# Kernel optimization log

Measured on AMD Instinct MI355X. Metric: run time of the kernel, lower is better.

Reference implementation:

```python
import jax, jax.numpy as jnp
import numpy as np

B, N, D = 2, 2048, 1024
H, QH, DH = 8, 16, 64        # kv heads, query heads, head dim
SOFTCLAMP = 50.0


def setup_inputs() -> dict:
    key = jax.random.key(0)
    ks = jax.random.split(key, 7)
    return {
        "tokens": jax.random.normal(ks[0], (B, N, D), jnp.float32),
        "norm_w": jnp.ones((D,), jnp.float32) + 0.02 * jax.random.normal(ks[1], (D,), jnp.float32),
        "Wq":  0.02 * jax.random.normal(ks[2], (D, QH * DH), jnp.float32),
        "Wkv": 0.02 * jax.random.normal(ks[3], (D, 2 * H * DH), jnp.float32),
        "Wout": 0.02 * jax.random.normal(ks[4], (H * DH, D), jnp.float32),
        "q_gamma": 0.02 * jax.random.normal(ks[5], (QH, DH), jnp.float32),
        "k_gamma": 0.02 * jax.random.normal(ks[6], (H, DH), jnp.float32),
    }


def _rmsnorm(x, w):
    eps = jnp.finfo(x.dtype).eps
    return x * jax.lax.rsqrt(jnp.mean(x * x, axis=-1, keepdims=True) + eps) * w


def _l2norm(x):
    # F.normalize(dim=-1, p=2) clamps the norm at eps=1e-12
    n = jnp.maximum(jnp.linalg.norm(x, axis=-1, keepdims=True), 1e-12)
    return x / n


def _mh_rmsnorm(x, gamma):
    # x: [b, h, n, d]; gamma: [h, d]; scale = (gamma + 1) * sqrt(d)
    scale = (gamma + 1.0) * np.sqrt(x.shape[-1]).astype(np.float32)
    return _l2norm(x) * scale[None, :, None, :]


def reference(tokens, norm_w, Wq, Wkv, Wout, q_gamma, k_gamma):
    b, n, d = tokens.shape
    x = _rmsnorm(tokens, norm_w)

    q = (x @ Wq).reshape(b, n, QH, DH).transpose(0, 2, 1, 3)      # [b, QH, n, dh]
    kv = x @ Wkv
    k = kv[..., : H * DH].reshape(b, n, H, DH).transpose(0, 2, 1, 3)  # [b, H, n, dh]
    v = kv[..., H * DH:].reshape(b, n, H, DH).transpose(0, 2, 1, 3)   # [b, H, n, dh]

    q = _mh_rmsnorm(q, q_gamma)
    k = _mh_rmsnorm(k, k_gamma)

    g = QH // H
    q = q.reshape(b, H, g, n, DH)                                 # [b, h, g, i, dh]

    sim = jnp.einsum('bhgid,bhjd->bhgij', q, k)                   # [b, h, g, i, j]
    sim = jnp.tanh(sim / SOFTCLAMP) * SOFTCLAMP                   # softcap BEFORE scale (faithful)
    sim = sim * (DH ** -0.5)

    neg = -jnp.finfo(sim.dtype).max
    causal = jnp.triu(jnp.ones((n, n), dtype=bool), 1)
    sim = jnp.where(causal, neg, sim)

    attn = jax.nn.softmax(sim, axis=-1)
    # NOTE: original einsum sums over the group axis g -> [b, h, i, dh]
    out = jnp.einsum('bhgij,bhjd->bhid', attn, v)
    out = out.transpose(0, 2, 1, 3).reshape(b, n, H * DH)
    return out @ Wout
```

## Files before the change

### kernel.cpp

```cpp
#include <hip/hip_runtime.h>
#include <hip/hip_bf16.h>
#include <type_traits>

typedef unsigned short u16;
typedef __attribute__((ext_vector_type(2))) float f32x2;
typedef __attribute__((ext_vector_type(4))) float f32x4;
typedef __attribute__((ext_vector_type(8))) short short8;
typedef __attribute__((ext_vector_type(4))) short short4v;
typedef __attribute__((ext_vector_type(8))) __bf16 bf16x8;
typedef __attribute__((ext_vector_type(4))) __bf16 bf16x4;

#define BB 2
#define NN 2048
#define DDIM 1024
#define HH 8
#define QHH 16
#define DHH 64

__device__ __forceinline__ float b2f(u16 v) {
    return __builtin_bit_cast(float, ((unsigned)v) << 16);
}
__device__ __forceinline__ u16 f2b(float f) {
    unsigned u = __builtin_bit_cast(unsigned, f);
    u += 0x7FFFu + ((u >> 16) & 1u);
    return (u16)(u >> 16);
}
__device__ __forceinline__ float fastrcp(float x) {
#if __has_builtin(__builtin_amdgcn_rcpf)
    return __builtin_amdgcn_rcpf(x);
#else
    return 1.0f / x;
#endif
}
__device__ __forceinline__ float fastexp2(float x) {
#if __has_builtin(__builtin_amdgcn_exp2f)
    return __builtin_amdgcn_exp2f(x);
#else
    return exp2f(x);
#endif
}
__device__ __forceinline__ f32x2 sp2(float v) { return (f32x2){v, v}; }
__device__ __forceinline__ f32x4 mfma16(short8 a, short8 b, f32x4 c) {
    return __builtin_amdgcn_mfma_f32_16x16x32_bf16(
        __builtin_bit_cast(bf16x8, a), __builtin_bit_cast(bf16x8, b), c, 0, 0, 0);
}
#if __has_builtin(__builtin_amdgcn_mfma_f32_16x16x16_bf16)
__device__ __forceinline__ f32x4 mfma_k16(short4v a, short4v b, f32x4 c) {
    return __builtin_amdgcn_mfma_f32_16x16x16_bf16(
        __builtin_bit_cast(bf16x4, a), __builtin_bit_cast(bf16x4, b), c, 0, 0, 0);
}
#else
__device__ __forceinline__ f32x4 mfma_k16(short4v a, short4v b, f32x4 c) {
    return __builtin_amdgcn_mfma_f32_16x16x16bf16_1k(a, b, c, 0, 0, 0);
}
#endif
__device__ __forceinline__ void stage16(const u16* g, u16* l, int lane) {
#if __has_builtin(__builtin_amdgcn_global_load_lds)
    __builtin_amdgcn_global_load_lds(
        (const __attribute__((address_space(1))) unsigned int*)g,
        (__attribute__((address_space(3))) unsigned int*)l, 16, 0, 0);
#else
    *(short8*)(l + lane * 8) = *(const short8*)g;
#endif
}

__global__ __launch_bounds__(256) void k_pre(const float* __restrict__ tokens,
                                             const float* __restrict__ norm_w,
                                             u16* __restrict__ xb,
                                             const float* __restrict__ Wq,
                                             const float* __restrict__ Wkv,
                                             const float* __restrict__ Wout,
                                             u16* __restrict__ WqT,
                                             u16* __restrict__ WkvT,
                                             u16* __restrict__ WoutT) {
    __shared__ float red[4];
    __shared__ u16 tile[32][33];
    const int bid = blockIdx.x;
    const int tid = threadIdx.x;
    if (bid < 4096) {
        const int row = bid;
        const float* xp = tokens + (size_t)row * DDIM + tid * 4;
        float4 raw = *(const float4*)xp;
        float ss = raw.x * raw.x + raw.y * raw.y + raw.z * raw.z + raw.w * raw.w;
#pragma unroll
        for (int d = 1; d < 64; d <<= 1) ss += __shfl_xor(ss, d);
        if ((tid & 63) == 0) red[tid >> 6] = ss;
        __syncthreads();
        float tot = red[0] + red[1] + red[2] + red[3];
        float r = rsqrtf(tot * (1.0f / 1024.0f) + 1.1920929e-7f);
        float4 wv = *(const float4*)(norm_w + tid * 4);
        ushort4 o;
        o.x = f2b(raw.x * r * wv.x);
        o.y = f2b(raw.y * r * wv.y);
        o.z = f2b(raw.z * r * wv.z);
        o.w = f2b(raw.w * r * wv.w);
        *(ushort4*)(xb + (size_t)row * DDIM + tid * 4) = o;
    } else {
        const int idx = bid - 4096;
        const int z = idx >> 10;
        const int rem = idx & 1023;
        const int by = rem >> 5, bx = rem & 31;
        const float* in = (z == 0) ? Wq : (z == 1) ? Wkv : Wout;
        u16* out = (z == 0) ? WqT : (z == 1) ? WkvT : WoutT;
        const int R = (z == 2) ? 512 : 1024, C = 1024;
        const int br = by * 32;
        if (br >= R) return;
        const int bc = bx * 32;
        const int tx = tid & 31, ty = tid >> 5;
#pragma unroll
        for (int i = 0; i < 32; i += 8)
            tile[ty + i][tx] = f2b(in[(size_t)(br + ty + i) * C + bc + tx]);
        __syncthreads();
#pragma unroll
        for (int i = 0; i < 32; i += 8)
            out[(size_t)(bc + ty + i) * R + br + tx] = tile[tx][ty + i];
    }
}

__global__ __launch_bounds__(256) void k_gemm128(const u16* __restrict__ A,
                                                 const u16* __restrict__ Bt,
                                                 u16* __restrict__ C,
                                                 int M, int Ncols, int K) {
    __shared__ __attribute__((aligned(16))) u16 As[128 * 64];
    __shared__ __attribute__((aligned(16))) u16 Bs[128 * 64];
    const int tid = threadIdx.x;
    const int lane = tid & 63;
    const int w = tid >> 6;
    const int i = blockIdx.y * 16 + blockIdx.x;
    const int xcd = i & 7, j = i >> 3;
    const int rm = xcd >> 1, rn = xcd & 1;
    const int m0 = (rm * 8 + (j >> 3)) * 128;
    const int n0 = (rn * 8 + (j & 7)) * 128;
    const int wr = (w >> 1) * 64;
    const int wc = (w & 1) * 64;
    const int lr = lane & 15;
    const int lq = lane >> 4;

    const int ch0 = w * 32;
    const int srow = lane >> 3;
    const int sch = (lane ^ srow) & 7;
    const u16* aSrc = A + (size_t)(m0 + ch0 + srow) * K + sch * 8;
    const u16* bSrc = Bt + (size_t)(n0 + ch0 + srow) * K + sch * 8;
    u16* aDst = As + ch0 * 64;
    u16* bDst = Bs + ch0 * 64;

    f32x4 acc[4][4];
#pragma unroll
    for (int i2 = 0; i2 < 4; i2++)
#pragma unroll
        for (int j2 = 0; j2 < 4; j2++) acc[i2][j2] = (f32x4){0.f, 0.f, 0.f, 0.f};

    for (int k0 = 0; k0 < K; k0 += 64) {
        __syncthreads();
#pragma unroll
        for (int c = 0; c < 4; ++c) {
            stage16(aSrc + (size_t)(c * 8) * K, aDst + c * 8 * 64, lane);
            stage16(bSrc + (size_t)(c * 8) * K, bDst + c * 8 * 64, lane);
        }
        aSrc += 64;
        bSrc += 64;
        __syncthreads();
#pragma unroll
        for (int kk = 0; kk < 2; ++kk) {
            short8 a[4], b[4];
#pragma unroll
            for (int mi = 0; mi < 4; ++mi) {
                const int row = wr + mi * 16 + lr;
                a[mi] = *(const short8*)&As[row * 64 + ((((kk << 2) + lq) ^ (lr & 7)) << 3)];
            }
#pragma unroll
            for (int ni = 0; ni < 4; ++ni) {
                const int row = wc + ni * 16 + lr;
                b[ni] = *(const short8*)&Bs[row * 64 + ((((kk << 2) + lq) ^ (lr & 7)) << 3)];
            }
#pragma unroll
            for (int mi = 0; mi < 4; ++mi)
#pragma unroll
                for (int ni = 0; ni < 4; ++ni) acc[mi][ni] = mfma16(a[mi], b[ni], acc[mi][ni]);
        }
    }
#pragma unroll
    for (int mi = 0; mi < 4; ++mi)
#pragma unroll
        for (int ni = 0; ni < 4; ++ni)
#pragma unroll
            for (int r = 0; r < 4; ++r) {
                int row = m0 + wr + mi * 16 + lq * 4 + r;
                int col = n0 + wc + ni * 16 + lr;
                C[(size_t)row * Ncols + col] = f2b(acc[mi][ni][r]);
            }
}

__global__ __launch_bounds__(256) void k_gemm64f(const u16* __restrict__ A,
                                                 const u16* __restrict__ Bt,
                                                 float* __restrict__ C,
                                                 int M, int Ncols, int K) {
    __shared__ __attribute__((aligned(16))) u16 As[64 * 64];
    __shared__ __attribute__((aligned(16))) u16 Bs[128 * 64];
    const int tid = threadIdx.x;
    const int lane = tid & 63;
    const int w = tid >> 6;
    const int m0 = blockIdx.y * 64;
    const int n0 = blockIdx.x * 128;
    const int lr = lane & 15;
    const int lq = lane >> 4;

    const int srow = lane >> 3;
    const int sch = (lane ^ srow) & 7;
    const u16* aSrc = A + (size_t)(m0 + w * 16 + srow) * K + sch * 8;
    const u16* bSrc = Bt + (size_t)(n0 + w * 32 + srow) * K + sch * 8;
    u16* aDst = As + w * 16 * 64;
    u16* bDst = Bs + w * 32 * 64;

    f32x4 acc[8];
#pragma unroll
    for (int i = 0; i < 8; i++) acc[i] = (f32x4){0.f, 0.f, 0.f, 0.f};

    for (int k0 = 0; k0 < K; k0 += 64) {
        __syncthreads();
#pragma unroll
        for (int c = 0; c < 2; ++c)
            stage16(aSrc + (size_t)(c * 8) * K, aDst + c * 8 * 64, lane);
#pragma unroll
        for (int c = 0; c < 4; ++c)
            stage16(bSrc + (size_t)(c * 8) * K, bDst + c * 8 * 64, lane);
        aSrc += 64;
        bSrc += 64;
        __syncthreads();
#pragma unroll
        for (int kk = 0; kk < 2; ++kk) {
            const int chunk = ((kk << 2) + lq) ^ (lr & 7);
            short8 a = *(const short8*)&As[(w * 16 + lr) * 64 + (chunk << 3)];
#pragma unroll
            for (int nt = 0; nt < 8; ++nt) {
                short8 b = *(const short8*)&Bs[(nt * 16 + lr) * 64 + (chunk << 3)];
                acc[nt] = mfma16(a, b, acc[nt]);
            }
        }
    }
#pragma unroll
    for (int nt = 0; nt < 8; ++nt)
#pragma unroll
        for (int r = 0; r < 4; ++r) {
            int row = m0 + w * 16 + lq * 4 + r;
            int col = n0 + nt * 16 + lr;
            C[(size_t)row * Ncols + col] = acc[nt][r];
        }
}

__global__ __launch_bounds__(256) void k_mid(const u16* __restrict__ qkv,
                                             const float* __restrict__ q_gamma,
                                             const float* __restrict__ k_gamma,
                                             u16* __restrict__ qn,
                                             u16* __restrict__ kn,
                                             u16* __restrict__ vt) {
    __shared__ u16 t[64 * 72];
    const int bid = blockIdx.x;
    const int tid = threadIdx.x;
    if (bid < 4096) {
        const int row = bid;
        const int b = row >> 11, n = row & 2047;
        const int lane = tid & 63, w = tid >> 6;
        const u16* qr = qkv + (size_t)row * 2048;
        const u16* kvr = qkv + (size_t)row * 2048 + 1024;
#pragma unroll
        for (int tq = 0; tq < 4; ++tq) {
            int qh = w * 4 + tq;
            float v = b2f(qr[qh * 64 + lane]);
            float ss = v * v;
#pragma unroll
            for (int d = 1; d < 64; d <<= 1) ss += __shfl_xor(ss, d);
            float nrm = fmaxf(sqrtf(ss), 1e-12f);
            float g = q_gamma[qh * 64 + lane];
            qn[((size_t)(b * QHH + qh) * NN + n) * 64 + lane] = f2b(v / nrm * (g + 1.0f) * 8.0f);
        }
#pragma unroll
        for (int tk = 0; tk < 2; ++tk) {
            int kh = w * 2 + tk;
            float v = b2f(kvr[kh * 64 + lane]);
            float ss = v * v;
#pragma unroll
            for (int d = 1; d < 64; d <<= 1) ss += __shfl_xor(ss, d);
            float nrm = fmaxf(sqrtf(ss), 1e-12f);
            float g = k_gamma[kh * 64 + lane];
            kn[((size_t)(b * HH + kh) * NN + n) * 64 + lane] = f2b(v / nrm * (g + 1.0f) * 0.16f);
        }
    } else {
        const int idx = bid - 4096;
        const int bh = idx & 15;
        const int b = bh >> 3, h = bh & 7;
        const int n0 = (idx >> 4) * 64;
#pragma unroll
        for (int it = 0; it < 2; ++it) {
            int id2 = tid + it * 256;
            int i = id2 >> 3, c = id2 & 7;
            short8 v = *(const short8*)&qkv[(size_t)(b * NN + n0 + i) * 2048 + 1536 + h * 64 + c * 8];
            *(short8*)&t[i * 72 + c * 8] = v;
        }
        __syncthreads();
#pragma unroll
        for (int it = 0; it < 2; ++it) {
            int id2 = tid + it * 256;
            int d = id2 >> 3, c = id2 & 7;
            const int sw = (d >> 3) & 1;
            u16 tmp[8], o[8];
#pragma unroll
            for (int j = 0; j < 8; ++j) tmp[j] = t[(c * 8 + j) * 72 + d];
#pragma unroll
            for (int j = 0; j < 8; ++j) o[j] = tmp[j ^ (sw << 2)];
            *(short8*)&vt[((size_t)(bh * 64 + d)) * NN + n0 + c * 8] = *(short8*)o;
        }
    }
}

__global__ __launch_bounds__(256) void k_attn(const u16* __restrict__ qn,
                                              const u16* __restrict__ kn,
                                              const u16* __restrict__ vt,
                                              u16* __restrict__ OT,
                                              float* __restrict__ Lp) {
    const int bq = blockIdx.x;
    const int b = bq >> 4, qh = bq & 15;
    const int h = qh >> 1;
    const int tid = threadIdx.x;
    const int lane = tid & 63, w = tid >> 6;
    const int lr = lane & 15, lq = lane >> 4;
    const int y = blockIdx.y;
    const int z = 31 - (y >> 1);
    const int s = y & 1;
    const int ntile = z + 1;
    const int jmid = (ntile + 1) >> 1;
    const int jb = s ? jmid : 0;
    const int je = s ? ntile : jmid;
    const int ntl = je - jb;
    const int i0 = z * 64 + w * 16;
    const int irow = i0 + lr;

    const u16* Qp = qn + (size_t)(b * QHH + qh) * NN * 64;
    const u16* Kp = kn + (size_t)(b * HH + h) * NN * 64;
    const u16* Vp = vt + (size_t)(b * HH + h) * 64 * NN;
    u16* Op = OT + (size_t)s * (BB * QHH * NN * 64) + (size_t)bq * NN * 64;
    float* Lsel = Lp + (size_t)s * (BB * QHH * NN) + (size_t)bq * NN;

    __shared__ __attribute__((aligned(16))) u16 Ks[64 * 64];
    __shared__ __attribute__((aligned(16))) u16 Vs[64 * 64];

    short8 qf0 = *(const short8*)&Qp[(size_t)(i0 + lr) * 64 + lq * 8];
    short8 qf1 = *(const short8*)&Qp[(size_t)(i0 + lr) * 64 + 32 + lq * 8];

    f32x4 of[4];
#pragma unroll
    for (int dt = 0; dt < 4; ++dt) of[dt] = (f32x4){0.f, 0.f, 0.f, 0.f};
    f32x2 ls = {0.f, 0.f};

    const int srow = lane >> 3;
    const int sch = (lane ^ srow) & 7;
    const int rA = w * 16, rB = w * 16 + 8;

    const u16* kSrcA = Kp + (size_t)jb * 4096 + (size_t)(rA + srow) * 64 + sch * 8;
    const u16* kSrcB = Kp + (size_t)jb * 4096 + (size_t)(rB + srow) * 64 + sch * 8;
    const u16* vSrcA = Vp + (size_t)(rA + srow) * NN + jb * 64 + sch * 8;
    const u16* vSrcB = Vp + (size_t)(rB + srow) * NN + jb * 64 + sch * 8;

    auto stageKV = [&]() {
        stage16(kSrcA, &Ks[rA * 64], lane);
        stage16(kSrcB, &Ks[rB * 64], lane);
        stage16(vSrcA, &Vs[rA * 64], lane);
        stage16(vSrcB, &Vs[rB * 64], lane);
        kSrcA += 64 * 64;
        kSrcB += 64 * 64;
        vSrcA += 64;
        vSrcB += 64;
    };

    auto smax = [&](f32x4 sc, int lim, bool masked) -> short4v {
        f32x2 xa = {sc[0], sc[1]};
        f32x2 xb = {sc[2], sc[3]};
        f32x2 ya = xa * xa;
        f32x2 yb = xb * xb;
        f32x2 Ga = __builtin_elementwise_fma(ya, __builtin_elementwise_fma(ya,
                       __builtin_elementwise_fma(ya, __builtin_elementwise_fma(ya,
                           sp2(0.04705711f), sp2(-0.32327190f)), sp2(1.11500760f)),
                       sp2(-2.98719110f)), sp2(9.01599730f));
        f32x2 Gb = __builtin_elementwise_fma(yb, __builtin_elementwise_fma(yb,
                       __builtin_elementwise_fma(yb, __builtin_elementwise_fma(yb,
                           sp2(0.04705711f), sp2(-0.32327190f)), sp2(1.11500760f)),
                       sp2(-2.98719110f)), sp2(9.01599730f));
        f32x2 aa = __builtin_elementwise_fma(xa, Ga, sp2(-9.0168440f));
        f32x2 ab = __builtin_elementwise_fma(xb, Gb, sp2(-9.0168440f));
        float p0 = fastexp2(aa.x);
        float p1 = fastexp2(aa.y);
        float p2 = fastexp2(ab.x);
        float p3 = fastexp2(ab.y);
        if (masked) {
            p0 = (0 <= lim) ? p0 : 0.0f;
            p1 = (1 <= lim) ? p1 : 0.0f;
            p2 = (2 <= lim) ? p2 : 0.0f;
            p3 = (3 <= lim) ? p3 : 0.0f;
        }
        ls += (f32x2){p0, p1};
        ls += (f32x2){p2, p3};
        bf16x4 pb;
        pb[0] = (__bf16)p0;
        pb[1] = (__bf16)p1;
        pb[2] = (__bf16)p2;
        pb[3] = (__bf16)p3;
        return __builtin_bit_cast(short4v, pb);
    };

    auto tile = [&](int jt) {
        const int j0 = jt << 6;
        const u16* kb = &Ks[0];
        const u16* vb = &Vs[0];
        f32x4 sc[4];
        __builtin_amdgcn_s_setprio(1);
#pragma unroll
        for (int ct = 0; ct < 4; ++ct) {
            const int r = ct * 16 + lr;
            short8 kf0 = *(const short8*)&kb[r * 64 + ((lq ^ (lr & 7)) << 3)];
            short8 kf1 = *(const short8*)&kb[r * 64 + (((4 + lq) ^ (lr & 7)) << 3)];
            f32x4 t = (f32x4){0.f, 0.f, 0.f, 0.f};
            t = mfma16(kf0, qf0, t);
            t = mfma16(kf1, qf1, t);
            sc[ct] = t;
        }
        __builtin_amdgcn_s_setprio(0);
        const bool masked = (jt == ntile - 1);
        short4v pk[4];
#pragma unroll
        for (int ct = 0; ct < 4; ++ct) {
            const int lim = irow - (j0 + ct * 16 + lq * 4);
            pk[ct] = smax(sc[ct], lim, masked);
        }
        __builtin_amdgcn_s_setprio(1);
#pragma unroll
        for (int dt = 0; dt < 4; ++dt) {
            const int d = dt * 16 + lr;
#pragma unroll
            for (int ct = 0; ct < 4; ++ct) {
                short4v vf = *(const short4v*)
                    &vb[d * 64 + ((((ct << 1) + (lq >> 1)) ^ (lr & 7)) << 3) +
                        (((lq ^ (lr >> 3)) & 1) << 2)];
                of[dt] = mfma_k16(vf, pk[ct], of[dt]);
            }
        }
        __builtin_amdgcn_s_setprio(0);
    };

    for (int t = 0; t < ntl; ++t) {
        __syncthreads();
        stageKV();
        __syncthreads();
        tile(jb + t);
    }

    float l = ls.x + ls.y;
    l += __shfl_xor(l, 16);
    l += __shfl_xor(l, 32);
#pragma unroll
    for (int dt = 0; dt < 4; ++dt) {
        u16 o[4];
#pragma unroll
        for (int r = 0; r < 4; ++r) o[r] = f2b(of[dt][r]);
        *(ushort4*)&Op[(size_t)irow * 64 + dt * 16 + lq * 4] = *(ushort4*)o;
    }
    if (lq == 0) Lsel[irow] = l;
}

__global__ __launch_bounds__(256) void k_gsum(const u16* __restrict__ O,
                                              const float* __restrict__ Lp,
                                              u16* __restrict__ AO) {
    const int idx = blockIdx.x * 256 + threadIdx.x;
    const int c8 = idx & 63;
    const int n = (idx >> 6) & 2047;
    const int b = idx >> 17;
    const int hh = c8 >> 3;
    const int ch = c8 & 7;
    const int q0 = b * QHH + 2 * hh, q1 = q0 + 1;
    const size_t SOFF = (size_t)BB * QHH * NN * 64;
    const size_t LOFF = (size_t)BB * QHH * NN;
    const u16* a0 = O + ((size_t)q0 * NN + n) * 64 + ch * 8;
    const u16* a1 = O + ((size_t)q1 * NN + n) * 64 + ch * 8;
    const u16* b0 = a0 + SOFF;
    const u16* b1 = a1 + SOFF;
    const float l0 = Lp[(size_t)q0 * NN + n] + Lp[LOFF + (size_t)q0 * NN + n];
    const float l1 = Lp[(size_t)q1 * NN + n] + Lp[LOFF + (size_t)q1 * NN + n];
    const float inv0 = fastrcp(l0);
    const float inv1 = fastrcp(l1);
    short8 va0 = *(const short8*)a0;
    short8 vb0 = *(const short8*)b0;
    short8 va1 = *(const short8*)a1;
    short8 vb1 = *(const short8*)b1;
    u16 o[8];
#pragma unroll
    for (int j = 0; j < 8; ++j)
        o[j] = f2b((b2f((u16)va0[j]) + b2f((u16)vb0[j])) * inv0 +
                   (b2f((u16)va1[j]) + b2f((u16)vb1[j])) * inv1);
    *(short8*)&AO[((size_t)(b * NN + n)) * 512 + c8 * 8] = *(short8*)o;
}

extern "C" void kernel_launch(void* const* d_in, const int* in_sizes, int n_in,
                              void* d_out, int out_size, void* d_ws, size_t ws_size,
                              hipStream_t stream) {
    const float* tokens = (const float*)d_in[0];
    const float* norm_w = (const float*)d_in[1];
    const float* Wq = (const float*)d_in[2];
    const float* Wkv = (const float*)d_in[3];
    const float* Wout = (const float*)d_in[4];
    const float* q_gamma = (const float*)d_in[5];
    const float* k_gamma = (const float*)d_in[6];
    float* out = (float*)d_out;

    char* ws = (char*)d_ws;
    u16* xb = (u16*)(ws + 0);
    u16* WqT = (u16*)(ws + 8388608);
    u16* WkvT = (u16*)(ws + 10485760);
    u16* WoutT = (u16*)(ws + 12582912);
    u16* qkv = (u16*)(ws + 13631488);
    u16* kn = (u16*)(ws + 30408704);
    u16* vtb = (u16*)(ws + 34603008);
    u16* qn = xb;
    u16* Opart = qkv;
    float* Lpart = (float*)(ws + 8388608);
    u16* AO = kn;

    k_pre<<<7168, 256, 0, stream>>>(tokens, norm_w, xb, Wq, Wkv, Wout, WqT, WkvT, WoutT);
    k_gemm128<<<dim3(16, 32), 256, 0, stream>>>(xb, WqT, qkv, 4096, 2048, 1024);
    k_mid<<<4608, 256, 0, stream>>>(qkv, q_gamma, k_gamma, qn, kn, vtb);
    k_attn<<<dim3(32, 64), 256, 0, stream>>>(qn, kn, vtb, Opart, Lpart);
    k_gsum<<<1024, 256, 0, stream>>>(Opart, Lpart, AO);
    k_gemm64f<<<dim3(8, 64), 256, 0, stream>>>(AO, WoutT, out, 4096, 1024, 512);
}
```

Before: 171.4 us.

## Fuse q/k head norm and V transpose into QKV GEMM epilogue

```diff
diff --git a/kernel.cpp b/kernel.cpp
--- a/kernel.cpp
+++ b/kernel.cpp
@@ -119,10 +119,15 @@
 
 __global__ __launch_bounds__(256) void k_gemm128(const u16* __restrict__ A,
                                                  const u16* __restrict__ Bt,
-                                                 u16* __restrict__ C,
-                                                 int M, int Ncols, int K) {
+                                                 const float* __restrict__ q_gamma,
+                                                 const float* __restrict__ k_gamma,
+                                                 u16* __restrict__ qn,
+                                                 u16* __restrict__ kn,
+                                                 u16* __restrict__ vt,
+                                                 int K) {
     __shared__ __attribute__((aligned(16))) u16 As[128 * 64];
     __shared__ __attribute__((aligned(16))) u16 Bs[128 * 64];
+    __shared__ __attribute__((aligned(16))) u16 Vst[4 * 64 * 72];
     const int tid = threadIdx.x;
     const int lane = tid & 63;
     const int w = tid >> 6;
@@ -179,16 +184,65 @@
                 for (int ni = 0; ni < 4; ++ni) acc[mi][ni] = mfma16(a[mi], b[ni], acc[mi][ni]);
         }
     }
-#pragma unroll
-    for (int mi = 0; mi < 4; ++mi)
-#pragma unroll
-        for (int ni = 0; ni < 4; ++ni)
+
+    const int colbase = n0 + wc;
+    if (colbase < 1536) {
+        const bool isQ = (colbase < 1024);
+        const int head = isQ ? (colbase >> 6) : ((colbase - 1024) >> 6);
+        const float* gamma = isQ ? q_gamma : k_gamma;
+        const float scl = isQ ? 8.0f : 0.16f;
+        u16* outp = isQ ? qn : kn;
+        const int HCNT = isQ ? QHH : HH;
+        float g[4];
+#pragma unroll
+        for (int ni = 0; ni < 4; ++ni) g[ni] = gamma[head * 64 + ni * 16 + lr] + 1.0f;
+#pragma unroll
+        for (int mi = 0; mi < 4; ++mi)
 #pragma unroll
             for (int r = 0; r < 4; ++r) {
-                int row = m0 + wr + mi * 16 + lq * 4 + r;
-                int col = n0 + wc + ni * 16 + lr;
-                C[(size_t)row * Ncols + col] = f2b(acc[mi][ni][r]);
+                float ss = 0.f;
+#pragma unroll
+                for (int ni = 0; ni < 4; ++ni)
+                    ss = fmaf(acc[mi][ni][r], acc[mi][ni][r], ss);
+                ss += __shfl_xor(ss, 1);
+                ss += __shfl_xor(ss, 2);
+                ss += __shfl_xor(ss, 4);
+                ss += __shfl_xor(ss, 8);
+                const float inv = scl / fmaxf(sqrtf(ss), 1e-12f);
+                const int m = m0 + wr + mi * 16 + lq * 4 + r;
+                const int b = m >> 11, n = m & 2047;
+                u16* rowp = outp + (((size_t)(b * HCNT + head) * NN + n) << 6);
+#pragma unroll
+                for (int ni = 0; ni < 4; ++ni)
+                    rowp[ni * 16 + lr] = f2b(acc[mi][ni][r] * inv * g[ni]);
             }
+    } else {
+        const int vh = (colbase - 1536) >> 6;
+        const int mbase = m0 + wr;
+        const int b = mbase >> 11, nb = mbase & 2047;
+        u16* sl = Vst + w * 64 * 72;
+#pragma unroll
+        for (int mi = 0; mi < 4; ++mi)
+#pragma unroll
+            for (int ni = 0; ni < 4; ++ni)
+#pragma unroll
+                for (int r = 0; r < 4; ++r)
+                    sl[(mi * 16 + lq * 4 + r) * 72 + ni * 16 + lr] = f2b(acc[mi][ni][r]);
+        __syncthreads();
+        u16* vrow = vt + ((size_t)(b * HH + vh) * 64) * NN;
+#pragma unroll
+        for (int it = 0; it < 8; ++it) {
+            int idx = it * 64 + lane;
+            int d = idx >> 3, c = idx & 7;
+            const int sw = (d >> 3) & 1;
+            u16 tmp[8], o[8];
+#pragma unroll
+            for (int jj = 0; jj < 8; ++jj) tmp[jj] = sl[(c * 8 + jj) * 72 + d];
+#pragma unroll
+            for (int jj = 0; jj < 8; ++jj) o[jj] = tmp[jj ^ (sw << 2)];
+            *(short8*)&vrow[(size_t)d * NN + nb + c * 8] = *(short8*)o;
+        }
+    }
 }
 
 __global__ __launch_bounds__(256) void k_gemm64f(const u16* __restrict__ A,
@@ -246,71 +300,6 @@
             int col = n0 + nt * 16 + lr;
             C[(size_t)row * Ncols + col] = acc[nt][r];
         }
-}
-
-__global__ __launch_bounds__(256) void k_mid(const u16* __restrict__ qkv,
-                                             const float* __restrict__ q_gamma,
-                                             const float* __restrict__ k_gamma,
-                                             u16* __restrict__ qn,
-                                             u16* __restrict__ kn,
-                                             u16* __restrict__ vt) {
-    __shared__ u16 t[64 * 72];
-    const int bid = blockIdx.x;
-    const int tid = threadIdx.x;
-    if (bid < 4096) {
-        const int row = bid;
-        const int b = row >> 11, n = row & 2047;
-        const int lane = tid & 63, w = tid >> 6;
-        const u16* qr = qkv + (size_t)row * 2048;
-        const u16* kvr = qkv + (size_t)row * 2048 + 1024;
-#pragma unroll
-        for (int tq = 0; tq < 4; ++tq) {
-            int qh = w * 4 + tq;
-            float v = b2f(qr[qh * 64 + lane]);
-            float ss = v * v;
-#pragma unroll
-            for (int d = 1; d < 64; d <<= 1) ss += __shfl_xor(ss, d);
-            float nrm = fmaxf(sqrtf(ss), 1e-12f);
-            float g = q_gamma[qh * 64 + lane];
-            qn[((size_t)(b * QHH + qh) * NN + n) * 64 + lane] = f2b(v / nrm * (g + 1.0f) * 8.0f);
-        }
-#pragma unroll
-        for (int tk = 0; tk < 2; ++tk) {
-            int kh = w * 2 + tk;
-            float v = b2f(kvr[kh * 64 + lane]);
-            float ss = v * v;
-#pragma unroll
-            for (int d = 1; d < 64; d <<= 1) ss += __shfl_xor(ss, d);
-            float nrm = fmaxf(sqrtf(ss), 1e-12f);
-            float g = k_gamma[kh * 64 + lane];
-            kn[((size_t)(b * HH + kh) * NN + n) * 64 + lane] = f2b(v / nrm * (g + 1.0f) * 0.16f);
-        }
-    } else {
-        const int idx = bid - 4096;
-        const int bh = idx & 15;
-        const int b = bh >> 3, h = bh & 7;
-        const int n0 = (idx >> 4) * 64;
-#pragma unroll
-        for (int it = 0; it < 2; ++it) {
-            int id2 = tid + it * 256;
-            int i = id2 >> 3, c = id2 & 7;
-            short8 v = *(const short8*)&qkv[(size_t)(b * NN + n0 + i) * 2048 + 1536 + h * 64 + c * 8];
-            *(short8*)&t[i * 72 + c * 8] = v;
-        }
-        __syncthreads();
-#pragma unroll
-        for (int it = 0; it < 2; ++it) {
-            int id2 = tid + it * 256;
-            int d = id2 >> 3, c = id2 & 7;
-            const int sw = (d >> 3) & 1;
-            u16 tmp[8], o[8];
-#pragma unroll
-            for (int j = 0; j < 8; ++j) tmp[j] = t[(c * 8 + j) * 72 + d];
-#pragma unroll
-            for (int j = 0; j < 8; ++j) o[j] = tmp[j ^ (sw << 2)];
-            *(short8*)&vt[((size_t)(bh * 64 + d)) * NN + n0 + c * 8] = *(short8*)o;
-        }
-    }
 }
 
 __global__ __launch_bounds__(256) void k_attn(const u16* __restrict__ qn,
@@ -515,17 +504,15 @@
     u16* WqT = (u16*)(ws + 8388608);
     u16* WkvT = (u16*)(ws + 10485760);
     u16* WoutT = (u16*)(ws + 12582912);
-    u16* qkv = (u16*)(ws + 13631488);
     u16* kn = (u16*)(ws + 30408704);
     u16* vtb = (u16*)(ws + 34603008);
-    u16* qn = xb;
-    u16* Opart = qkv;
+    u16* qn = (u16*)(ws + 38797312);
+    u16* Opart = (u16*)(ws + 13631488);
     float* Lpart = (float*)(ws + 8388608);
     u16* AO = kn;
 
     k_pre<<<7168, 256, 0, stream>>>(tokens, norm_w, xb, Wq, Wkv, Wout, WqT, WkvT, WoutT);
-    k_gemm128<<<dim3(16, 32), 256, 0, stream>>>(xb, WqT, qkv, 4096, 2048, 1024);
-    k_mid<<<4608, 256, 0, stream>>>(qkv, q_gamma, k_gamma, qn, kn, vtb);
+    k_gemm128<<<dim3(16, 32), 256, 0, stream>>>(xb, WqT, q_gamma, k_gamma, qn, kn, vtb, 1024);
     k_attn<<<dim3(32, 64), 256, 0, stream>>>(qn, kn, vtb, Opart, Lpart);
     k_gsum<<<1024, 256, 0, stream>>>(Opart, Lpart, AO);
     k_gemm64f<<<dim3(8, 64), 256, 0, stream>>>(AO, WoutT, out, 4096, 1024, 512);
```

After: 166.0 us. 3.2% less time.
